# Performance work log

Measured on AMD Instinct MI355X. Metric: run time of the kernel, lower is better.

The kernel has to match this reference:

```python
import jax, jax.numpy as jnp
import numpy as np

B, C, H, W = 256, 1024, 7, 7
D_HID, N_CLS = 768, 5

def setup_inputs() -> dict:
    key = jax.random.key(0)
    k1, k2, k3, k4, k5 = jax.random.split(key, 5)
    flat = C * H * W  # 50176
    return {
        "features": jax.random.normal(k1, (B, C, H, W), dtype=jnp.float32),
        "W1": jax.random.normal(k2, (D_HID, flat), dtype=jnp.float32) * 0.02,
        "b1": jax.random.normal(k3, (D_HID,), dtype=jnp.float32) * 0.02,
        "W2": jax.random.normal(k4, (N_CLS, D_HID), dtype=jnp.float32) * 0.02,
        "b2": jax.random.normal(k5, (N_CLS,), dtype=jnp.float32) * 0.02,
    }

def reference(features, W1, b1, W2, b2):
    # PCAM: per-(batch, channel) global max over spatial dims, broadcast-multiplied
    # back onto the feature map. Replaces the torch Python double loop with one
    # fused reduce-max + elementwise multiply.
    ch_max = jnp.max(features, axis=(2, 3), keepdims=True)  # [B, C, 1, 1]
    pcams = features * ch_max                               # [B, C, H, W]
    flat = pcams.reshape(pcams.shape[0], -1)                # [B, C*H*W]
    h = jax.nn.relu(flat @ W1.T + b1)                       # [B, 768]
    logits = h @ W2.T + b2                                  # [B, num_classes]
    return (logits, features)
```

## Files before the change

### kernel.cpp

```cpp
#include <hip/hip_runtime.h>
#include <hip/hip_bf16.h>

#define B_SZ   256
#define C_SZ   1024
#define HW     49
#define KDIM   50176
#define DHID   768
#define NCLS   5

typedef __bf16 bf16x8 __attribute__((ext_vector_type(8)));
typedef float  f32x4  __attribute__((ext_vector_type(4)));

#define BARRIER() do { \
    asm volatile("s_waitcnt lgkmcnt(0)" ::: "memory"); \
    __builtin_amdgcn_s_barrier(); \
    asm volatile("" ::: "memory"); \
  } while (0)

__global__ __launch_bounds__(256) void pcam_kernel(const float* __restrict__ feat,
                                                   float* __restrict__ feat_out,
                                                   __bf16* __restrict__ pcam) {
  __shared__ float sv[1568];
  __shared__ float smax[32];
  const int tid = threadIdx.x;
  const size_t base = (size_t)blockIdx.x * 1568;

  const float4* src4 = (const float4*)(feat + base);
  float4* dst4 = (float4*)(feat_out + base);
  #pragma unroll
  for (int i = 0; i < 2; ++i) {
    int idx = tid + i * 256;
    if (idx < 392) {
      float4 v = src4[idx];
      dst4[idx] = v;
      ((float4*)sv)[idx] = v;
    }
  }
  __syncthreads();

  {
    const int r = tid >> 3, p = tid & 7;
    float mx = -INFINITY;
    for (int i = p; i < HW; i += 8) mx = fmaxf(mx, sv[r * HW + i]);
    #pragma unroll
    for (int off = 1; off < 8; off <<= 1) mx = fmaxf(mx, __shfl_xor(mx, off));
    if (p == 0) smax[r] = mx;
  }
  __syncthreads();

  for (int i = tid; i < 1568; i += 256) {
    int r = (i * 1338) >> 16;
    float v = sv[i] * smax[r];
    pcam[base + i] = (__bf16)v;
  }
}

#define BM 256
#define BN 128
#define KC 64
#define NT 6
#define KSPLIT 42
#define KSTEPS 784

__global__ __launch_bounds__(512, 2) void gemm1_kernel(const __bf16* __restrict__ pcam,
                                                       const float* __restrict__ W1,
                                                       float* __restrict__ h_part) {
  __shared__ __bf16 Asm[2][BM * KC];

  const int tid  = threadIdx.x;
  const int lane = tid & 63;
  const int w    = tid >> 6;
  const int n0   = blockIdx.x * BN;
  const int ks   = blockIdx.y;
  const int s0   = (ks * KSTEPS) / KSPLIT;
  const int s1   = ((ks + 1) * KSTEPS) / KSPLIT;

  const float* bbase = W1 + (size_t)(n0 + w * 16 + (lane & 15)) * KDIM + (lane >> 4) * 8;

  unsigned a_off[4];
  int      a_lds[4];
  #pragma unroll
  for (int it = 0; it < 4; ++it) {
    const unsigned ug = it * 512 + tid;
    const unsigned m  = ug >> 3;
    const unsigned u  = ug & 7;
    a_off[it] = m * (unsigned)KDIM + ((u ^ (m & 7)) * 8u);
    a_lds[it] = (int)(ug * 8);
  }

  f32x4 acc[16];
  #pragma unroll
  for (int i = 0; i < 16; ++i) acc[i] = f32x4{0.f, 0.f, 0.f, 0.f};

  bf16x8 ar[4];

#define LOAD_A(s) do { \
    _Pragma("unroll") \
    for (int it = 0; it < 4; ++it) \
      ar[it] = *(const bf16x8*)(pcam + a_off[it] + (unsigned)(s) * KC); \
  } while (0)

#define WRITE_A(bi) do { \
    _Pragma("unroll") \
    for (int it = 0; it < 4; ++it) \
      *(bf16x8*)(&Asm[bi][a_lds[it]]) = ar[it]; \
  } while (0)

#define COMPUTE(bi, s) do { \
    _Pragma("unroll") \
    for (int ksub = 0; ksub < 2; ++ksub) { \
      const f32x4 v0 = *(const f32x4*)(bbase + (size_t)(s) * KC + ksub * 32); \
      const f32x4 v1 = *(const f32x4*)(bbase + (size_t)(s) * KC + ksub * 32 + 4); \
      bf16x8 bfr; \
      bfr[0] = (__bf16)v0[0]; bfr[1] = (__bf16)v0[1]; \
      bfr[2] = (__bf16)v0[2]; bfr[3] = (__bf16)v0[3]; \
      bfr[4] = (__bf16)v1[0]; bfr[5] = (__bf16)v1[1]; \
      bfr[6] = (__bf16)v1[2]; bfr[7] = (__bf16)v1[3]; \
      const int u = ksub * 4 + (lane >> 4); \
      _Pragma("unroll") \
      for (int i = 0; i < 16; ++i) { \
        const int m = i * 16 + (lane & 15); \
        const bf16x8 af = *(const bf16x8*)((const char*)Asm[bi] + m * 128 + ((u ^ (m & 7)) << 4)); \
        acc[i] = __builtin_amdgcn_mfma_f32_16x16x32_bf16(af, bfr, acc[i], 0, 0, 0); \
      } \
    } \
  } while (0)

  LOAD_A(s0);
  WRITE_A(0);
  BARRIER();

  for (int s = s0; s < s1; ++s) {
    const int cur = (s - s0) & 1;
    if (s + 1 < s1) LOAD_A(s + 1);
    COMPUTE(cur, s);
    if (s + 1 < s1) WRITE_A(cur ^ 1);
    BARRIER();
  }

  float* out = h_part + (size_t)ks * DHID * B_SZ;
  const int n = n0 + w * 16 + (lane & 15);
  #pragma unroll
  for (int i = 0; i < 16; ++i) {
    const int mb = i * 16 + (lane >> 4) * 4;
    *(f32x4*)(out + (size_t)n * B_SZ + mb) = acc[i];
  }
#undef LOAD_A
#undef WRITE_A
#undef COMPUTE
}

__global__ __launch_bounds__(256) void reduce_kernel(const float* __restrict__ h_part,
                                                     const float* __restrict__ b1,
                                                     float* __restrict__ h) {
  const int n = blockIdx.x;
  const int m = threadIdx.x;
  float s = 0.f;
  #pragma unroll 6
  for (int ks = 0; ks < KSPLIT; ++ks)
    s += h_part[((size_t)ks * DHID + n) * B_SZ + m];
  float v = s + b1[n];
  h[(size_t)m * DHID + n] = v > 0.f ? v : 0.f;
}

__global__ __launch_bounds__(64) void head_kernel(const float* __restrict__ h,
                                                  const float* __restrict__ W2,
                                                  const float* __restrict__ b2,
                                                  float* __restrict__ logits) {
  const int m = blockIdx.x;
  const int lane = threadIdx.x;
  float hv[12];
  #pragma unroll
  for (int j = 0; j < 12; ++j) hv[j] = h[(size_t)m * DHID + j * 64 + lane];
  #pragma unroll
  for (int c = 0; c < NCLS; ++c) {
    float s = 0.f;
    #pragma unroll
    for (int j = 0; j < 12; ++j) s += hv[j] * W2[c * DHID + j * 64 + lane];
    #pragma unroll
    for (int off = 32; off > 0; off >>= 1) s += __shfl_xor(s, off);
    if (lane == 0) logits[m * NCLS + c] = s + b2[c];
  }
}

extern "C" void kernel_launch(void* const* d_in, const int* in_sizes, int n_in,
                              void* d_out, int out_size, void* d_ws, size_t ws_size,
                              hipStream_t stream) {
  const float* feat = (const float*)d_in[0];
  const float* W1   = (const float*)d_in[1];
  const float* b1   = (const float*)d_in[2];
  const float* W2   = (const float*)d_in[3];
  const float* b2   = (const float*)d_in[4];

  float* logits   = (float*)d_out;
  float* feat_out = (float*)d_out + (size_t)B_SZ * NCLS;

  char* ws = (char*)d_ws;
  __bf16* pcam   = (__bf16*)ws;
  float*  h_part = (float*)(ws + (size_t)B_SZ * KDIM * 2);
  float*  h      = (float*)(ws + (size_t)B_SZ * KDIM * 2
                               + (size_t)KSPLIT * DHID * B_SZ * 4);

  pcam_kernel<<<(B_SZ * C_SZ) / 32, 256, 0, stream>>>(feat, feat_out, pcam);
  gemm1_kernel<<<dim3(NT, KSPLIT), 512, 0, stream>>>(pcam, W1, h_part);
  reduce_kernel<<<DHID, 256, 0, stream>>>(h_part, b1, h);
  head_kernel<<<B_SZ, 64, 0, stream>>>(h, W2, b2, logits);
}
```

Before: 103.9 us.

## Pipeline GEMM1 with direct global-to-LDS loads and deep W1 register prefetch

Rewrites the split-K GEMM main loop. A tiles are now loaded straight into a triple-buffered LDS ring with global_load_lds, which removes the register staging and LDS write step. W1 fragments are prefetched six steps ahead in registers, and the wait on memory counters is a vmcnt wait instead of a full lgkmcnt drain. BK drops to 32 and the swizzle changes to match. Launch bounds go to one block per CU, which risks lower occupancy, and the vmcnt(6) accounting is fragile.

```diff
diff --git a/kernel.cpp b/kernel.cpp
--- a/kernel.cpp
+++ b/kernel.cpp
@@ -11,11 +11,9 @@
 typedef __bf16 bf16x8 __attribute__((ext_vector_type(8)));
 typedef float  f32x4  __attribute__((ext_vector_type(4)));
 
-#define BARRIER() do { \
-    asm volatile("s_waitcnt lgkmcnt(0)" ::: "memory"); \
-    __builtin_amdgcn_s_barrier(); \
-    asm volatile("" ::: "memory"); \
-  } while (0)
+#define GLOAD_LDS16(gsrc, ldst) \
+  __builtin_amdgcn_global_load_lds((__attribute__((address_space(1))) void*)(gsrc), \
+                                   (__attribute__((address_space(3))) void*)(ldst), 16, 0, 0)
 
 __global__ __launch_bounds__(256) void pcam_kernel(const float* __restrict__ feat,
                                                    float* __restrict__ feat_out,
@@ -57,97 +55,97 @@
 
 #define BM 256
 #define BN 128
-#define KC 64
+#define BK 32
 #define NT 6
 #define KSPLIT 42
-#define KSTEPS 784
-
-__global__ __launch_bounds__(512, 2) void gemm1_kernel(const __bf16* __restrict__ pcam,
+#define KSTEPS 1568
+
+__global__ __launch_bounds__(512, 1) void gemm1_kernel(const __bf16* __restrict__ pcam,
                                                        const float* __restrict__ W1,
                                                        float* __restrict__ h_part) {
-  __shared__ __bf16 Asm[2][BM * KC];
+  __shared__ __bf16 Asm[3][BM * BK];
 
   const int tid  = threadIdx.x;
   const int lane = tid & 63;
   const int w    = tid >> 6;
+  const int c_   = lane & 15;
   const int n0   = blockIdx.x * BN;
   const int ks   = blockIdx.y;
   const int s0   = (ks * KSTEPS) / KSPLIT;
   const int s1   = ((ks + 1) * KSTEPS) / KSPLIT;
 
-  const float* bbase = W1 + (size_t)(n0 + w * 16 + (lane & 15)) * KDIM + (lane >> 4) * 8;
-
-  unsigned a_off[4];
-  int      a_lds[4];
-  #pragma unroll
-  for (int it = 0; it < 4; ++it) {
-    const unsigned ug = it * 512 + tid;
-    const unsigned m  = ug >> 3;
-    const unsigned u  = ug & 7;
-    a_off[it] = m * (unsigned)KDIM + ((u ^ (m & 7)) * 8u);
-    a_lds[it] = (int)(ug * 8);
-  }
+  const float* bbase = W1 + (size_t)(n0 + w * 16 + c_) * KDIM + (lane >> 4) * 8;
+
+  unsigned a_off0, a_off1;
+  {
+    unsigned ug, m;
+    ug = (w * 2 + 0) * 64 + lane; m = ug >> 2;
+    a_off0 = m * (unsigned)KDIM + (((ug & 3) ^ (m & 3)) * 8u);
+    ug = (w * 2 + 1) * 64 + lane; m = ug >> 2;
+    a_off1 = m * (unsigned)KDIM + (((ug & 3) ^ (m & 3)) * 8u);
+  }
+  const int uoff = (((lane >> 4) ^ (lane & 3)) << 4);
 
   f32x4 acc[16];
   #pragma unroll
   for (int i = 0; i < 16; ++i) acc[i] = f32x4{0.f, 0.f, 0.f, 0.f};
 
-  bf16x8 ar[4];
-
-#define LOAD_A(s) do { \
-    _Pragma("unroll") \
-    for (int it = 0; it < 4; ++it) \
-      ar[it] = *(const bf16x8*)(pcam + a_off[it] + (unsigned)(s) * KC); \
-  } while (0)
-
-#define WRITE_A(bi) do { \
-    _Pragma("unroll") \
-    for (int it = 0; it < 4; ++it) \
-      *(bf16x8*)(&Asm[bi][a_lds[it]]) = ar[it]; \
-  } while (0)
-
-#define COMPUTE(bi, s) do { \
-    _Pragma("unroll") \
-    for (int ksub = 0; ksub < 2; ++ksub) { \
-      const f32x4 v0 = *(const f32x4*)(bbase + (size_t)(s) * KC + ksub * 32); \
-      const f32x4 v1 = *(const f32x4*)(bbase + (size_t)(s) * KC + ksub * 32 + 4); \
-      bf16x8 bfr; \
-      bfr[0] = (__bf16)v0[0]; bfr[1] = (__bf16)v0[1]; \
-      bfr[2] = (__bf16)v0[2]; bfr[3] = (__bf16)v0[3]; \
-      bfr[4] = (__bf16)v1[0]; bfr[5] = (__bf16)v1[1]; \
-      bfr[6] = (__bf16)v1[2]; bfr[7] = (__bf16)v1[3]; \
-      const int u = ksub * 4 + (lane >> 4); \
+  f32x4 q0a, q0b, q1a, q1b, q2a, q2b, q3a, q3b, q4a, q4b, q5a, q5b;
+
+  GLOAD_LDS16(pcam + a_off0 + (unsigned)s0 * BK, (char*)Asm[0] + (w * 2 + 0) * 1024);
+  GLOAD_LDS16(pcam + a_off1 + (unsigned)s0 * BK, (char*)Asm[0] + (w * 2 + 1) * 1024);
+  GLOAD_LDS16(pcam + a_off0 + (unsigned)(s0 + 1) * BK, (char*)Asm[1] + (w * 2 + 0) * 1024);
+  GLOAD_LDS16(pcam + a_off1 + (unsigned)(s0 + 1) * BK, (char*)Asm[1] + (w * 2 + 1) * 1024);
+  q0a = *(const f32x4*)(bbase + (size_t)(s0 + 0) * BK); q0b = *(const f32x4*)(bbase + (size_t)(s0 + 0) * BK + 4);
+  q1a = *(const f32x4*)(bbase + (size_t)(s0 + 1) * BK); q1b = *(const f32x4*)(bbase + (size_t)(s0 + 1) * BK + 4);
+  q2a = *(const f32x4*)(bbase + (size_t)(s0 + 2) * BK); q2b = *(const f32x4*)(bbase + (size_t)(s0 + 2) * BK + 4);
+  q3a = *(const f32x4*)(bbase + (size_t)(s0 + 3) * BK); q3b = *(const f32x4*)(bbase + (size_t)(s0 + 3) * BK + 4);
+  q4a = *(const f32x4*)(bbase + (size_t)(s0 + 4) * BK); q4b = *(const f32x4*)(bbase + (size_t)(s0 + 4) * BK + 4);
+  q5a = *(const f32x4*)(bbase + (size_t)(s0 + 5) * BK); q5b = *(const f32x4*)(bbase + (size_t)(s0 + 5) * BK + 4);
+
+#define STEPQ(JI, QA, QB) do { \
+    const int t = s0 + jo * 6 + (JI); \
+    asm volatile("s_waitcnt vmcnt(6)" ::: "memory"); \
+    __builtin_amdgcn_s_barrier(); \
+    const bool act = (t < s1); \
+    bf16x8 bfr; \
+    if (act) { \
+      bfr[0] = (__bf16)QA[0]; bfr[1] = (__bf16)QA[1]; bfr[2] = (__bf16)QA[2]; bfr[3] = (__bf16)QA[3]; \
+      bfr[4] = (__bf16)QB[0]; bfr[5] = (__bf16)QB[1]; bfr[6] = (__bf16)QB[2]; bfr[7] = (__bf16)QB[3]; \
+    } \
+    { const int ta = (t + 2 < s1) ? (t + 2) : (s1 - 1); \
+      GLOAD_LDS16(pcam + a_off0 + (unsigned)ta * BK, (char*)Asm[((JI) + 2) % 3] + (w * 2 + 0) * 1024); \
+      GLOAD_LDS16(pcam + a_off1 + (unsigned)ta * BK, (char*)Asm[((JI) + 2) % 3] + (w * 2 + 1) * 1024); \
+      const int tb = (t + 6 < s1) ? (t + 6) : (s1 - 1); \
+      QA = *(const f32x4*)(bbase + (size_t)tb * BK); \
+      QB = *(const f32x4*)(bbase + (size_t)tb * BK + 4); } \
+    if (act) { \
       _Pragma("unroll") \
       for (int i = 0; i < 16; ++i) { \
-        const int m = i * 16 + (lane & 15); \
-        const bf16x8 af = *(const bf16x8*)((const char*)Asm[bi] + m * 128 + ((u ^ (m & 7)) << 4)); \
+        const int m = i * 16 + c_; \
+        const bf16x8 af = *(const bf16x8*)((const char*)Asm[(JI) % 3] + m * 64 + uoff); \
         acc[i] = __builtin_amdgcn_mfma_f32_16x16x32_bf16(af, bfr, acc[i], 0, 0, 0); \
       } \
     } \
   } while (0)
 
-  LOAD_A(s0);
-  WRITE_A(0);
-  BARRIER();
-
-  for (int s = s0; s < s1; ++s) {
-    const int cur = (s - s0) & 1;
-    if (s + 1 < s1) LOAD_A(s + 1);
-    COMPUTE(cur, s);
-    if (s + 1 < s1) WRITE_A(cur ^ 1);
-    BARRIER();
-  }
+  for (int jo = 0; jo < 7; ++jo) {
+    STEPQ(0, q0a, q0b);
+    STEPQ(1, q1a, q1b);
+    STEPQ(2, q2a, q2b);
+    STEPQ(3, q3a, q3b);
+    STEPQ(4, q4a, q4b);
+    STEPQ(5, q5a, q5b);
+  }
+#undef STEPQ
 
   float* out = h_part + (size_t)ks * DHID * B_SZ;
-  const int n = n0 + w * 16 + (lane & 15);
+  const int n = n0 + w * 16 + c_;
   #pragma unroll
   for (int i = 0; i < 16; ++i) {
     const int mb = i * 16 + (lane >> 4) * 4;
     *(f32x4*)(out + (size_t)n * B_SZ + mb) = acc[i];
   }
-#undef LOAD_A
-#undef WRITE_A
-#undef COMPUTE
 }
 
 __global__ __launch_bounds__(256) void reduce_kernel(const float* __restrict__ h_part,
```

Result: faster. 98.40 us (-5.3%).

## Stage GEMM tiles via direct global-to-LDS loads and store split-K partials in bf16

Applied to the files above, without the earlier changes.

The A tile now moves from global memory straight into LDS with global_load_lds, issued two steps ahead. W1 is loaded once per block as fp32, converted to bf16 and staged in swizzled LDS, where before each wave converted it inside the MFMA loop. Split-K partial sums are written as bf16 to halve the partial-buffer traffic into the reduce kernel. Launch bounds drop to one block per CU for the larger LDS footprint, and bf16 partials lose accuracy in the final sum.

```diff
diff --git a/kernel.cpp b/kernel.cpp
--- a/kernel.cpp
+++ b/kernel.cpp
@@ -9,7 +9,12 @@
 #define NCLS   5
 
 typedef __bf16 bf16x8 __attribute__((ext_vector_type(8)));
+typedef __bf16 bf16x4 __attribute__((ext_vector_type(4)));
 typedef float  f32x4  __attribute__((ext_vector_type(4)));
+
+#define GLOAD_LDS16(gsrc, ldst) \
+  __builtin_amdgcn_global_load_lds((__attribute__((address_space(1))) void*)(gsrc), \
+                                   (__attribute__((address_space(3))) void*)(ldst), 16, 0, 0)
 
 #define BARRIER() do { \
     asm volatile("s_waitcnt lgkmcnt(0)" ::: "memory"); \
@@ -57,100 +62,129 @@
 
 #define BM 256
 #define BN 128
-#define KC 64
+#define BK 64
 #define NT 6
 #define KSPLIT 42
 #define KSTEPS 784
 
-__global__ __launch_bounds__(512, 2) void gemm1_kernel(const __bf16* __restrict__ pcam,
+__global__ __launch_bounds__(512, 1) void gemm1_kernel(const __bf16* __restrict__ pcam,
                                                        const float* __restrict__ W1,
-                                                       float* __restrict__ h_part) {
-  __shared__ __bf16 Asm[2][BM * KC];
+                                                       __bf16* __restrict__ h_part) {
+  __shared__ __bf16 Asm[2][BM * BK];
+  __shared__ __bf16 Bsm[2][BN * BK];
 
   const int tid  = threadIdx.x;
   const int lane = tid & 63;
   const int w    = tid >> 6;
+  const int c_   = lane & 15;
+  const int q_   = lane >> 4;
   const int n0   = blockIdx.x * BN;
   const int ks   = blockIdx.y;
   const int s0   = (ks * KSTEPS) / KSPLIT;
   const int s1   = ((ks + 1) * KSTEPS) / KSPLIT;
 
-  const float* bbase = W1 + (size_t)(n0 + w * 16 + (lane & 15)) * KDIM + (lane >> 4) * 8;
-
   unsigned a_off[4];
-  int      a_lds[4];
   #pragma unroll
   for (int it = 0; it < 4; ++it) {
     const unsigned ug = it * 512 + tid;
     const unsigned m  = ug >> 3;
-    const unsigned u  = ug & 7;
-    a_off[it] = m * (unsigned)KDIM + ((u ^ (m & 7)) * 8u);
-    a_lds[it] = (int)(ug * 8);
-  }
+    a_off[it] = m * (unsigned)KDIM + (((ug & 7) ^ (m & 7)) * 8u);
+  }
+
+  const float* bsrc[4];
+  #pragma unroll
+  for (int i = 0; i < 4; ++i)
+    bsrc[i] = W1 + (size_t)(n0 + w * 16 + i * 4 + q_) * KDIM + c_ * 4;
+
+  int bwr[4];
+  #pragma unroll
+  for (int i = 0; i < 4; ++i) {
+    const int r = w * 16 + i * 4 + q_;
+    bwr[i] = r * 128 + (((c_ >> 1) ^ (r & 7)) << 4) + ((c_ & 1) << 3);
+  }
+  const int rn = w * 16 + c_;
 
   f32x4 acc[16];
   #pragma unroll
   for (int i = 0; i < 16; ++i) acc[i] = f32x4{0.f, 0.f, 0.f, 0.f};
 
-  bf16x8 ar[4];
-
-#define LOAD_A(s) do { \
+  f32x4 bq0, bq1, bq2, bq3;
+
+#define ISSUE_A(bi, s) do { \
+    const unsigned ka = (unsigned)(s) * BK; \
     _Pragma("unroll") \
     for (int it = 0; it < 4; ++it) \
-      ar[it] = *(const bf16x8*)(pcam + a_off[it] + (unsigned)(s) * KC); \
-  } while (0)
-
-#define WRITE_A(bi) do { \
+      GLOAD_LDS16(pcam + a_off[it] + ka, (char*)Asm[bi] + it * 8192 + w * 1024); \
+  } while (0)
+
+#define ISSUE_B(s) do { \
+    const size_t kb = (size_t)(s) * BK; \
+    bq0 = *(const f32x4*)(bsrc[0] + kb); \
+    bq1 = *(const f32x4*)(bsrc[1] + kb); \
+    bq2 = *(const f32x4*)(bsrc[2] + kb); \
+    bq3 = *(const f32x4*)(bsrc[3] + kb); \
+  } while (0)
+
+#define WRITE_B(bi) do { \
     _Pragma("unroll") \
-    for (int it = 0; it < 4; ++it) \
-      *(bf16x8*)(&Asm[bi][a_lds[it]]) = ar[it]; \
-  } while (0)
-
-#define COMPUTE(bi, s) do { \
+    for (int i = 0; i < 4; ++i) { \
+      const f32x4 v = (i == 0) ? bq0 : (i == 1) ? bq1 : (i == 2) ? bq2 : bq3; \
+      bf16x4 bv; \
+      bv[0] = (__bf16)v[0]; bv[1] = (__bf16)v[1]; \
+      bv[2] = (__bf16)v[2]; bv[3] = (__bf16)v[3]; \
+      *(bf16x4*)((char*)Bsm[bi] + bwr[i]) = bv; \
+    } \
+  } while (0)
+
+#define COMPUTE(bi) do { \
     _Pragma("unroll") \
     for (int ksub = 0; ksub < 2; ++ksub) { \
-      const f32x4 v0 = *(const f32x4*)(bbase + (size_t)(s) * KC + ksub * 32); \
-      const f32x4 v1 = *(const f32x4*)(bbase + (size_t)(s) * KC + ksub * 32 + 4); \
-      bf16x8 bfr; \
-      bfr[0] = (__bf16)v0[0]; bfr[1] = (__bf16)v0[1]; \
-      bfr[2] = (__bf16)v0[2]; bfr[3] = (__bf16)v0[3]; \
-      bfr[4] = (__bf16)v1[0]; bfr[5] = (__bf16)v1[1]; \
-      bfr[6] = (__bf16)v1[2]; bfr[7] = (__bf16)v1[3]; \
-      const int u = ksub * 4 + (lane >> 4); \
+      const int u = ksub * 4 + q_; \
+      const bf16x8 bfr = *(const bf16x8*)((const char*)Bsm[bi] + rn * 128 + ((u ^ (rn & 7)) << 4)); \
       _Pragma("unroll") \
       for (int i = 0; i < 16; ++i) { \
-        const int m = i * 16 + (lane & 15); \
+        const int m = i * 16 + c_; \
         const bf16x8 af = *(const bf16x8*)((const char*)Asm[bi] + m * 128 + ((u ^ (m & 7)) << 4)); \
         acc[i] = __builtin_amdgcn_mfma_f32_16x16x32_bf16(af, bfr, acc[i], 0, 0, 0); \
       } \
     } \
   } while (0)
 
-  LOAD_A(s0);
-  WRITE_A(0);
+  ISSUE_A(0, s0);
+  ISSUE_B(s0);
+  asm volatile("s_waitcnt vmcnt(0)" ::: "memory");
+  WRITE_B(0);
   BARRIER();
+  if (s0 + 1 < s1) { ISSUE_A(1, s0 + 1); ISSUE_B(s0 + 1); }
 
   for (int s = s0; s < s1; ++s) {
     const int cur = (s - s0) & 1;
-    if (s + 1 < s1) LOAD_A(s + 1);
-    COMPUTE(cur, s);
-    if (s + 1 < s1) WRITE_A(cur ^ 1);
+    COMPUTE(cur);
+    if (s + 1 < s1) {
+      asm volatile("s_waitcnt vmcnt(0)" ::: "memory");
+      WRITE_B(cur ^ 1);
+    }
     BARRIER();
-  }
-
-  float* out = h_part + (size_t)ks * DHID * B_SZ;
-  const int n = n0 + w * 16 + (lane & 15);
+    if (s + 2 < s1) { ISSUE_A(cur, s + 2); ISSUE_B(s + 2); }
+  }
+
+  __bf16* out = h_part + (size_t)ks * DHID * B_SZ;
+  const int n = n0 + w * 16 + c_;
   #pragma unroll
   for (int i = 0; i < 16; ++i) {
-    const int mb = i * 16 + (lane >> 4) * 4;
-    *(f32x4*)(out + (size_t)n * B_SZ + mb) = acc[i];
-  }
-#undef LOAD_A
-#undef WRITE_A
+    const int mb = i * 16 + q_ * 4;
+    bf16x4 pv;
+    pv[0] = (__bf16)acc[i][0]; pv[1] = (__bf16)acc[i][1];
+    pv[2] = (__bf16)acc[i][2]; pv[3] = (__bf16)acc[i][3];
+    *(bf16x4*)(out + (size_t)n * B_SZ + mb) = pv;
+  }
+#undef ISSUE_A
+#undef ISSUE_B
+#undef WRITE_B
 #undef COMPUTE
 }
 
-__global__ __launch_bounds__(256) void reduce_kernel(const float* __restrict__ h_part,
+__global__ __launch_bounds__(256) void reduce_kernel(const __bf16* __restrict__ h_part,
                                                      const float* __restrict__ b1,
                                                      float* __restrict__ h) {
   const int n = blockIdx.x;
@@ -158,7 +192,7 @@
   float s = 0.f;
   #pragma unroll 6
   for (int ks = 0; ks < KSPLIT; ++ks)
-    s += h_part[((size_t)ks * DHID + n) * B_SZ + m];
+    s += (float)h_part[((size_t)ks * DHID + n) * B_SZ + m];
   float v = s + b1[n];
   h[(size_t)m * DHID + n] = v > 0.f ? v : 0.f;
 }
@@ -197,9 +231,9 @@
 
   char* ws = (char*)d_ws;
   __bf16* pcam   = (__bf16*)ws;
-  float*  h_part = (float*)(ws + (size_t)B_SZ * KDIM * 2);
+  __bf16* h_part = (__bf16*)(ws + (size_t)B_SZ * KDIM * 2);
   float*  h      = (float*)(ws + (size_t)B_SZ * KDIM * 2
-                               + (size_t)KSPLIT * DHID * B_SZ * 4);
+                               + (size_t)KSPLIT * DHID * B_SZ * 2);
 
   pcam_kernel<<<(B_SZ * C_SZ) / 32, 256, 0, stream>>>(feat, feat_out, pcam);
   gemm1_kernel<<<dim3(NT, KSPLIT), 512, 0, stream>>>(pcam, W1, h_part);
```

Result: faster. 93.93 us (-9.6%).
